# Kernel tuning notes

Hardware: AMD Instinct MI355X
Metric: run time of the kernel (lower is better)

## Reference

```python
import jax, jax.numpy as jnp
import numpy as np

L, D, H, FF, P, IMG, B = 6, 1024, 16, 4096, 14, 224, 16
S = (IMG // P) ** 2 + 1  # 257 tokens (CLS + patches)
DH = D // H
TOPK_RATIO, MOD_START, MOD_END = 0.8, 3, -2
EPS = 1e-5


def _ln(x, w, b):
    m = x.mean(-1, keepdims=True)
    v = ((x - m) ** 2).mean(-1, keepdims=True)
    return (x - m) * jax.lax.rsqrt(v + EPS) * w + b


def _quick_gelu(x):
    return x * jax.nn.sigmoid(1.702 * x)


def setup_inputs() -> dict:
    key = jax.random.key(0)
    ks = jax.random.split(key, 16)
    w = 0.02
    inp = {
        "pixel_values": jax.random.normal(ks[0], (B, 3, IMG, IMG), jnp.float32),
        "patch_w": jax.random.normal(ks[1], (D, 3, P, P), jnp.float32) * w,
        "class_emb": jax.random.normal(ks[2], (D,), jnp.float32) * w,
        "pos_emb": jax.random.normal(ks[3], (S, D), jnp.float32) * w,
        "ln1_w": jnp.ones((L, D), jnp.float32),
        "ln1_b": jnp.zeros((L, D), jnp.float32),
        "q_w": jax.random.normal(ks[4], (L, D, D), jnp.float32) * w,
        "q_b": jnp.zeros((L, D), jnp.float32),
        "k_w": jax.random.normal(ks[5], (L, D, D), jnp.float32) * w,
        "k_b": jnp.zeros((L, D), jnp.float32),
        "v_w": jax.random.normal(ks[6], (L, D, D), jnp.float32) * w,
        "v_b": jnp.zeros((L, D), jnp.float32),
        "o_w": jax.random.normal(ks[7], (L, D, D), jnp.float32) * w,
        "o_b": jnp.zeros((L, D), jnp.float32),
        "ln2_w": jnp.ones((L, D), jnp.float32),
        "ln2_b": jnp.zeros((L, D), jnp.float32),
        "fc1_w": jax.random.normal(ks[8], (L, FF, D), jnp.float32) * w,
        "fc1_b": jnp.zeros((L, FF), jnp.float32),
        "fc2_w": jax.random.normal(ks[9], (L, D, FF), jnp.float32) * w,
        "fc2_b": jnp.zeros((L, D), jnp.float32),
    }
    return inp


def reference(pixel_values, patch_w, class_emb, pos_emb,
              ln1_w, ln1_b, q_w, q_b, k_w, k_b, v_w, v_b, o_w, o_b,
              ln2_w, ln2_b, fc1_w, fc1_b, fc2_w, fc2_b):
    # --- CLIP vision embeddings (note: custom forward skips pre_layrnorm) ---
    feats = jax.lax.conv_general_dilated(
        pixel_values, patch_w, (P, P), 'VALID',
        dimension_numbers=('NCHW', 'OIHW', 'NCHW'))  # [B, D, 16, 16]
    feats = feats.reshape(B, D, -1).transpose(0, 2, 1)  # [B, 256, D]
    cls = jnp.broadcast_to(class_emb, (B, 1, D))
    x = jnp.concatenate([cls, feats], axis=1) + pos_emb[None]  # [B, S, D]

    scale = DH ** -0.5
    top_k = int(S * TOPK_RATIO)

    for idx in range(L):
        # --- CLIP encoder layer (pre-LN) ---
        res = x
        h = _ln(x, ln1_w[idx], ln1_b[idx])
        q = (h @ q_w[idx].T + q_b[idx]).reshape(B, S, H, DH)
        k = (h @ k_w[idx].T + k_b[idx]).reshape(B, S, H, DH)
        v = (h @ v_w[idx].T + v_b[idx]).reshape(B, S, H, DH)
        scores = jnp.einsum('bqhd,bkhd->bhqk', q, k) * scale
        attn = jax.nn.softmax(scores, axis=-1)  # [B, H, S, S]
        ctx = jnp.einsum('bhqk,bkhd->bqhd', attn, v).reshape(B, S, D)
        x = res + (ctx @ o_w[idx].T + o_b[idx])
        res = x
        h = _ln(x, ln2_w[idx], ln2_b[idx])
        h = _quick_gelu(h @ fc1_w[idx].T + fc1_b[idx])
        x = res + (h @ fc2_w[idx].T + fc2_b[idx])

        # --- MoD-style top-k selection + per-batch mask scatter ---
        if MOD_START <= idx <= L + MOD_END and (idx - MOD_START) % 2 == 0:
            aw = attn.mean(axis=1)                 # [B, S, S]
            sc = aw.sum(axis=2)                    # [B, S]
            sc = sc / sc.sum(axis=1, keepdims=True)
            _, top_idx = jax.lax.top_k(sc, top_k)  # [B, top_k]
            mask = jnp.zeros((B, S), bool).at[jnp.arange(B)[:, None], top_idx].set(True)
            # Original torch loop writes hidden_states back into a clone on both
            # mask and ~mask -> mathematically an identity copy.
            x = jnp.where(mask[:, :, None], x, x)

    return x


if __name__ == '__main__':
    out = reference(**setup_inputs())
    print(out.shape, out.dtype)
```

## Files before the change

### kernel.cpp

```cpp
#include <hip/hip_runtime.h>
#include <stdint.h>

typedef uint16_t u16;
typedef __attribute__((ext_vector_type(8))) short short8;
typedef __attribute__((ext_vector_type(4))) float f32x4;
typedef __attribute__((ext_vector_type(4))) u16 u16x4;

__device__ __forceinline__ u16 f2bf(float f) {
  union { float f; uint32_t i; } v; v.f = f;
  uint32_t r = v.i + 0x7fffu + ((v.i >> 16) & 1u);
  return (u16)(r >> 16);
}
__device__ __forceinline__ int imin(int a, int b) { return a < b ? a : b; }

#define GLD_LDS(gp, lp) __builtin_amdgcn_global_load_lds( \
    (__attribute__((address_space(1))) void*)(uintptr_t)(gp), \
    (__attribute__((address_space(3))) void*)(lp), 16, 0, 0)

#define BATCH 16
#define SEQ 257
#define DIM 1024
#define HEADS 16
#define DHEAD 64
#define FFDIM 4096
#define MROWS (BATCH * SEQ)
#define SPAD 288
#define KC 608

enum { EPI_PATCH = 0, EPI_QKV = 1, EPI_RES = 2, EPI_GELU = 3 };

struct GemmP {
  const u16* A; const u16* B;
  const float* bias;
  int lda, ldb, M, N, K;
  void* out;
  void* out2; void* out3;
  const float* aux;
};

template <int EPI, int MT>
__global__ __launch_bounds__(256) void gemm_bt(GemmP p) {
  constexpr int TM = MT * 32;
  constexpr int AISS = MT / 2;
  __shared__ __align__(16) u16 sA[TM * 32];
  __shared__ __align__(16) u16 sB[128 * 32];
  const int tid = threadIdx.x;
  const int w = tid >> 6, l = tid & 63, quad = l >> 4, lr = l & 15;
  const int wr = w >> 1, wc = w & 1;
  const int m0 = blockIdx.y * TM, n0 = blockIdx.x * 128;

  long aoff[AISS];
#pragma unroll
  for (int i = 0; i < AISS; ++i) {
    const int f = tid + i * 256;
    aoff[i] = (long)imin(m0 + (f >> 2), p.M - 1) * p.lda + ((f & 3) << 3);
  }
  long boff[2];
#pragma unroll
  for (int i = 0; i < 2; ++i) {
    const int f = tid + i * 256;
    boff[i] = (long)imin(n0 + (f >> 2), p.N - 1) * p.ldb + ((f & 3) << 3);
  }

  f32x4 acc[MT][4];
#pragma unroll
  for (int i = 0; i < MT; ++i)
#pragma unroll
    for (int j = 0; j < 4; ++j) acc[i][j] = (f32x4){0.f, 0.f, 0.f, 0.f};

  for (int k0 = 0; k0 < p.K; k0 += 32) {
    __syncthreads();
#pragma unroll
    for (int i = 0; i < AISS; ++i)
      GLD_LDS(p.A + aoff[i] + k0, &sA[(tid + i * 256) * 8]);
#pragma unroll
    for (int i = 0; i < 2; ++i)
      GLD_LDS(p.B + boff[i] + k0, &sB[(tid + i * 256) * 8]);
    __syncthreads();
    short8 af[MT], bg[4];
#pragma unroll
    for (int t = 0; t < MT; ++t)
      af[t] = *(const short8*)&sA[(wr * (MT * 16) + t * 16 + lr) * 32 + quad * 8];
#pragma unroll
    for (int t = 0; t < 4; ++t)
      bg[t] = *(const short8*)&sB[(wc * 64 + t * 16 + lr) * 32 + quad * 8];
#pragma unroll
    for (int mt = 0; mt < MT; ++mt)
#pragma unroll
      for (int nt = 0; nt < 4; ++nt)
        acc[mt][nt] = __builtin_amdgcn_mfma_f32_16x16x32_bf16(af[mt], bg[nt], acc[mt][nt], 0, 0, 0);
  }

#pragma unroll
  for (int mt = 0; mt < MT; ++mt) {
#pragma unroll
    for (int r = 0; r < 4; ++r) {
      const int gm = m0 + wr * (MT * 16) + mt * 16 + quad * 4 + r;
      if (gm >= p.M) continue;
#pragma unroll
      for (int nt = 0; nt < 4; ++nt) {
        const int gn = n0 + wc * 64 + nt * 16 + lr;
        if (gn >= p.N) continue;
        float v = acc[mt][nt][r];
        if (p.bias) v += p.bias[gn];
        if constexpr (EPI == EPI_PATCH) {
          const int b = gm >> 8, pp = gm & 255;
          ((float*)p.out)[((long)(b * SEQ + 1 + pp)) * DIM + gn] =
              v + p.aux[(1 + pp) * DIM + gn];
        } else if constexpr (EPI == EPI_QKV) {
          const int b = gm / SEQ, s = gm % SEQ;
          const int seg = gn >> 10, dloc = gn & 1023;
          const int h = dloc >> 6, dd = dloc & 63;
          const u16 val = f2bf(v);
          if (seg == 0)
            ((u16*)p.out)[(((long)(b * HEADS + h) * SEQ + s)) * DHEAD + dd] = val;
          else if (seg == 1)
            ((u16*)p.out2)[(((long)(b * HEADS + h) * SEQ + s)) * DHEAD + dd] = val;
          else
            ((u16*)p.out3)[((long)(b * HEADS + h) * DHEAD + dd) * SPAD + s] = val;
        } else if constexpr (EPI == EPI_RES) {
          float* o = (float*)p.out;
          o[(long)gm * p.N + gn] += v;
        } else if constexpr (EPI == EPI_GELU) {
          const float g = v / (1.f + __expf(-1.702f * v));
          ((u16*)p.out)[(long)gm * p.N + gn] = f2bf(g);
        }
      }
    }
  }
}

__global__ __launch_bounds__(256) void ln_k(const float* __restrict__ X,
                                            const float* __restrict__ w,
                                            const float* __restrict__ b,
                                            u16* __restrict__ O) {
  const int row = blockIdx.x, tid = threadIdx.x;
  const float4* xr = (const float4*)(X + (long)row * DIM);
  float4 v = xr[tid];
  float s = v.x + v.y + v.z + v.w;
  float s2 = v.x * v.x + v.y * v.y + v.z * v.z + v.w * v.w;
  for (int o = 32; o; o >>= 1) { s += __shfl_xor(s, o); s2 += __shfl_xor(s2, o); }
  __shared__ float red[8];
  const int wv = tid >> 6, l = tid & 63;
  if (l == 0) { red[wv] = s; red[4 + wv] = s2; }
  __syncthreads();
  s = red[0] + red[1] + red[2] + red[3];
  s2 = red[4] + red[5] + red[6] + red[7];
  const float mean = s * (1.f / DIM);
  const float var = s2 * (1.f / DIM) - mean * mean;
  const float rs = rsqrtf(var + 1e-5f);
  const int c = tid * 4;
  const float4 wv4 = *(const float4*)(w + c);
  const float4 bv4 = *(const float4*)(b + c);
  u16x4 o4;
  o4.x = f2bf((v.x - mean) * rs * wv4.x + bv4.x);
  o4.y = f2bf((v.y - mean) * rs * wv4.y + bv4.y);
  o4.z = f2bf((v.z - mean) * rs * wv4.z + bv4.z);
  o4.w = f2bf((v.w - mean) * rs * wv4.w + bv4.w);
  *(u16x4*)(O + (long)row * DIM + c) = o4;
}

__global__ __launch_bounds__(256) void attn_k(const u16* __restrict__ Q,
                                              const u16* __restrict__ Kx,
                                              const u16* __restrict__ Vt,
                                              u16* __restrict__ Ctx) {
  const int bh = blockIdx.x;
  const int q0 = blockIdx.y * 16;
  __shared__ float S[16][292];
  __shared__ __align__(16) u16 P[16][SPAD];
  const int tid = threadIdx.x, w = tid >> 6, l = tid & 63, quad = l >> 4, lr = l & 15;
  const u16* Qb = Q + (long)bh * SEQ * DHEAD;
  const u16* Kb = Kx + (long)bh * SEQ * DHEAD;
  const u16* Vb = Vt + (long)bh * DHEAD * SPAD;
  int qm = q0 + lr; if (qm > SEQ - 1) qm = SEQ - 1;
  const short8 aq0 = *(const short8*)(Qb + qm * DHEAD + quad * 8);
  const short8 aq1 = *(const short8*)(Qb + qm * DHEAD + 32 + quad * 8);
  for (int ct = 0; ct < 5; ++ct) {
    const int cn = ct * 64 + w * 16 + lr;
    const int cc = cn > SEQ - 1 ? SEQ - 1 : cn;
    const short8 b0 = *(const short8*)(Kb + cc * DHEAD + quad * 8);
    const short8 b1 = *(const short8*)(Kb + cc * DHEAD + 32 + quad * 8);
    f32x4 acc = (f32x4){0.f, 0.f, 0.f, 0.f};
    acc = __builtin_amdgcn_mfma_f32_16x16x32_bf16(aq0, b0, acc, 0, 0, 0);
    acc = __builtin_amdgcn_mfma_f32_16x16x32_bf16(aq1, b1, acc, 0, 0, 0);
    if (cn < SEQ) {
#pragma unroll
      for (int r = 0; r < 4; ++r) S[quad * 4 + r][cn] = acc[r] * 0.125f;
    }
  }
  __syncthreads();
#pragma unroll
  for (int rr = 0; rr < 4; ++rr) {
    const int m = w * 4 + rr;
    float mx = -1e30f;
    for (int c = l; c < SEQ; c += 64) mx = fmaxf(mx, S[m][c]);
    for (int o = 32; o; o >>= 1) mx = fmaxf(mx, __shfl_xor(mx, o));
    float sum = 0.f;
    for (int c = l; c < SEQ; c += 64) {
      const float e = __expf(S[m][c] - mx);
      S[m][c] = e;
      sum += e;
    }
    for (int o = 32; o; o >>= 1) sum += __shfl_xor(sum, o);
    const float inv = 1.f / sum;
    for (int c = l; c < SPAD; c += 64) P[m][c] = (c < SEQ) ? f2bf(S[m][c] * inv) : (u16)0;
  }
  __syncthreads();
  f32x4 acc = (f32x4){0.f, 0.f, 0.f, 0.f};
  for (int k0 = 0; k0 < SPAD; k0 += 32) {
    const short8 ap = *(const short8*)&P[lr][k0 + quad * 8];
    const short8 bv = *(const short8*)(Vb + (long)(w * 16 + lr) * SPAD + k0 + quad * 8);
    acc = __builtin_amdgcn_mfma_f32_16x16x32_bf16(ap, bv, acc, 0, 0, 0);
  }
  const int b = bh >> 4, h = bh & 15;
#pragma unroll
  for (int r = 0; r < 4; ++r) {
    const int q = q0 + quad * 4 + r;
    if (q < SEQ)
      Ctx[((long)(b * SEQ + q)) * DIM + h * DHEAD + w * 16 + lr] = f2bf(acc[r]);
  }
}

__global__ void f2b_k(const float* __restrict__ src, u16* __restrict__ dst, int n4) {
  const int i = blockIdx.x * 256 + threadIdx.x;
  if (i >= n4) return;
  const float4 v = ((const float4*)src)[i];
  u16x4 o;
  o.x = f2bf(v.x); o.y = f2bf(v.y); o.z = f2bf(v.z); o.w = f2bf(v.w);
  ((u16x4*)dst)[i] = o;
}

__global__ void cat3_k(const float* __restrict__ a, const float* __restrict__ b,
                       const float* __restrict__ c, float* __restrict__ o) {
  const int i = blockIdx.x * 256 + threadIdx.x;
  o[i] = (i < 1024) ? a[i] : (i < 2048 ? b[i - 1024] : c[i - 2048]);
}

__global__ void im2col_k(const float* __restrict__ pv, u16* __restrict__ out) {
  const long i = (long)blockIdx.x * 256 + threadIdx.x;
  if (i >= (long)4096 * KC) return;
  const int col = (int)(i % KC);
  const long row = i / KC;
  u16 val = 0;
  if (col < 588) {
    const int b = (int)(row >> 8), p = (int)(row & 255);
    const int py = p >> 4, px = p & 15;
    const int c = col / 196, rem = col % 196;
    const int ky = rem / 14, kx = rem % 14;
    val = f2bf(pv[(((long)b * 3 + c) * 224 + (py * 14 + ky)) * 224 + (px * 14 + kx)]);
  }
  out[i] = val;
}

__global__ void pwpad_k(const float* __restrict__ pw, u16* __restrict__ out) {
  const int i = blockIdx.x * 256 + threadIdx.x;
  if (i >= DIM * KC) return;
  const int col = i % KC, row = i / KC;
  out[i] = (col < 588) ? f2bf(pw[row * 588 + col]) : (u16)0;
}

__global__ void cls_k(const float* __restrict__ cls, const float* __restrict__ pos,
                      float* __restrict__ X) {
  const int i = blockIdx.x * 256 + threadIdx.x;
  const int b = i >> 10, d = i & 1023;
  X[((long)b * SEQ) * DIM + d] = cls[d] + pos[d];
}

__global__ void vtpad_k(u16* __restrict__ Vt) {
  const int i = blockIdx.x * 256 + threadIdx.x;
  if (i >= 256 * 64 * 31) return;
  const int dall = i / 31, s = SEQ + i % 31;
  Vt[(long)dall * SPAD + s] = 0;
}

__global__ void out_k(const float* __restrict__ X, float* __restrict__ O) {
  const int i = blockIdx.x * 256 + threadIdx.x;
  ((float4*)O)[i] = ((const float4*)X)[i];
}

#define OFF_X 0L
#define OFF_H 16842752L
#define OFF_Q 25264128L
#define OFF_K 33685504L
#define OFF_VT 42106880L
#define OFF_CTX 51544064L
#define OFF_FF 59965440L
#define OFF_W 93650944L
#define OFF_B3 (OFF_W + 6291456L)
#define OFF_IM OFF_FF
#define OFF_PW (OFF_FF + 4980736L)

extern "C" void kernel_launch(void* const* d_in, const int* in_sizes, int n_in,
                              void* d_out, int out_size, void* d_ws, size_t ws_size,
                              hipStream_t stream) {
  const float* pv = (const float*)d_in[0];
  const float* patch_w = (const float*)d_in[1];
  const float* class_emb = (const float*)d_in[2];
  const float* pos_emb = (const float*)d_in[3];
  const float* ln1_w = (const float*)d_in[4];
  const float* ln1_b = (const float*)d_in[5];
  const float* q_w = (const float*)d_in[6];
  const float* q_b = (const float*)d_in[7];
  const float* k_w = (const float*)d_in[8];
  const float* k_b = (const float*)d_in[9];
  const float* v_w = (const float*)d_in[10];
  const float* v_b = (const float*)d_in[11];
  const float* o_w = (const float*)d_in[12];
  const float* o_b = (const float*)d_in[13];
  const float* ln2_w = (const float*)d_in[14];
  const float* ln2_b = (const float*)d_in[15];
  const float* fc1_w = (const float*)d_in[16];
  const float* fc1_b = (const float*)d_in[17];
  const float* fc2_w = (const float*)d_in[18];
  const float* fc2_b = (const float*)d_in[19];

  char* ws = (char*)d_ws;
  float* X = (float*)(ws + OFF_X);
  u16* Hb = (u16*)(ws + OFF_H);
  u16* Qb = (u16*)(ws + OFF_Q);
  u16* Kb = (u16*)(ws + OFF_K);
  u16* Vt = (u16*)(ws + OFF_VT);
  u16* Ctx = (u16*)(ws + OFF_CTX);
  u16* FFh = (u16*)(ws + OFF_FF);
  u16* Wb = (u16*)(ws + OFF_W);
  float* B3 = (float*)(ws + OFF_B3);
  u16* Im = (u16*)(ws + OFF_IM);
  u16* Pw = (u16*)(ws + OFF_PW);

  const int NSQ4 = DIM * DIM / 4;
  const int NFF4 = FFDIM * DIM / 4;
  const int GSQ = (NSQ4 + 255) / 256, GFF = (NFF4 + 255) / 256;

  im2col_k<<<(4096 * KC + 255) / 256, 256, 0, stream>>>(pv, Im);
  pwpad_k<<<(DIM * KC + 255) / 256, 256, 0, stream>>>(patch_w, Pw);
  cls_k<<<(BATCH * DIM) / 256, 256, 0, stream>>>(class_emb, pos_emb, X);
  vtpad_k<<<(256 * 64 * 31 + 255) / 256, 256, 0, stream>>>(Vt);
  {
    GemmP g = {};
    g.A = Im; g.lda = KC; g.B = Pw; g.ldb = KC; g.bias = nullptr;
    g.M = 4096; g.N = DIM; g.K = KC; g.out = X; g.aux = pos_emb;
    gemm_bt<EPI_PATCH, 2><<<dim3(8, 64, 1), 256, 0, stream>>>(g);
  }

  for (int idx = 0; idx < 6; ++idx) {
    ln_k<<<MROWS, 256, 0, stream>>>(X, ln1_w + idx * DIM, ln1_b + idx * DIM, Hb);
    {
      f2b_k<<<GSQ, 256, 0, stream>>>(q_w + (long)idx * DIM * DIM, Wb, NSQ4);
      f2b_k<<<GSQ, 256, 0, stream>>>(k_w + (long)idx * DIM * DIM, Wb + DIM * DIM, NSQ4);
      f2b_k<<<GSQ, 256, 0, stream>>>(v_w + (long)idx * DIM * DIM, Wb + 2 * DIM * DIM, NSQ4);
      cat3_k<<<12, 256, 0, stream>>>(q_b + idx * DIM, k_b + idx * DIM, v_b + idx * DIM, B3);
      GemmP g = {};
      g.A = Hb; g.lda = DIM; g.B = Wb; g.ldb = DIM; g.bias = B3;
      g.M = MROWS; g.N = 3 * DIM; g.K = DIM;
      g.out = Qb; g.out2 = Kb; g.out3 = Vt;
      gemm_bt<EPI_QKV, 4><<<dim3(24, 33, 1), 256, 0, stream>>>(g);
    }
    attn_k<<<dim3(256, 17, 1), 256, 0, stream>>>(Qb, Kb, Vt, Ctx);
    {
      GemmP g = {};
      f2b_k<<<GSQ, 256, 0, stream>>>(o_w + (long)idx * DIM * DIM, Wb, NSQ4);
      g.A = Ctx; g.lda = DIM; g.B = Wb; g.ldb = DIM;
      g.bias = o_b + idx * DIM; g.M = MROWS; g.N = DIM; g.K = DIM; g.out = X;
      gemm_bt<EPI_RES, 2><<<dim3(8, 65, 1), 256, 0, stream>>>(g);
    }
    ln_k<<<MROWS, 256, 0, stream>>>(X, ln2_w + idx * DIM, ln2_b + idx * DIM, Hb);
    {
      GemmP g = {};
      f2b_k<<<GFF, 256, 0, stream>>>(fc1_w + (long)idx * FFDIM * DIM, Wb, NFF4);
      g.A = Hb; g.lda = DIM; g.B = Wb; g.ldb = DIM;
      g.bias = fc1_b + idx * FFDIM; g.M = MROWS; g.N = FFDIM; g.K = DIM; g.out = FFh;
      gemm_bt<EPI_GELU, 4><<<dim3(32, 33, 1), 256, 0, stream>>>(g);
    }
    {
      GemmP g = {};
      f2b_k<<<GFF, 256, 0, stream>>>(fc2_w + (long)idx * DIM * FFDIM, Wb, NFF4);
      g.A = FFh; g.lda = FFDIM; g.B = Wb; g.ldb = FFDIM;
      g.bias = fc2_b + idx * DIM; g.M = MROWS; g.N = DIM; g.K = FFDIM; g.out = X;
      gemm_bt<EPI_RES, 2><<<dim3(8, 65, 1), 256, 0, stream>>>(g);
    }
  }
  out_k<<<(MROWS * DIM / 4) / 256, 256, 0, stream>>>(X, (float*)d_out);
}
```

Measured before the change: 2.571 ms.

## Double GEMM K-step to 64 with two-panel LDS tiles; fuse QKV weight conversion

The GEMM main loop now loads a 64-wide K slab per iteration, stored as two 32-column panels in shared memory, and issues two MFMAs per accumulator between barriers. This halves the number of barrier pairs and load-issue rounds per K, at the cost of doubled LDS use, which may reduce occupancy. The patch-embedding K padding grows from 608 to 640 so it divides by 64, which adds a little extra zero work. The three separate Q/K/V weight conversion launches are merged into a single kernel.

New measurement: 2.560 ms. Within noise of the previous version (-0.5%).

```diff
diff --git a/kernel.cpp b/kernel.cpp
--- a/kernel.cpp
+++ b/kernel.cpp
@@ -25,7 +25,7 @@
 #define FFDIM 4096
 #define MROWS (BATCH * SEQ)
 #define SPAD 288
-#define KC 608
+#define KC 640
 
 enum { EPI_PATCH = 0, EPI_QKV = 1, EPI_RES = 2, EPI_GELU = 3 };
 
@@ -41,25 +41,28 @@
 template <int EPI, int MT>
 __global__ __launch_bounds__(256) void gemm_bt(GemmP p) {
   constexpr int TM = MT * 32;
-  constexpr int AISS = MT / 2;
-  __shared__ __align__(16) u16 sA[TM * 32];
-  __shared__ __align__(16) u16 sB[128 * 32];
+  constexpr int NA = TM / 32;
+  constexpr int SHA = (MT == 4) ? 9 : 8;
+  __shared__ __align__(16) u16 sA[2][TM][32];
+  __shared__ __align__(16) u16 sB[2][128][32];
   const int tid = threadIdx.x;
   const int w = tid >> 6, l = tid & 63, quad = l >> 4, lr = l & 15;
   const int wr = w >> 1, wc = w & 1;
   const int m0 = blockIdx.y * TM, n0 = blockIdx.x * 128;
 
-  long aoff[AISS];
-#pragma unroll
-  for (int i = 0; i < AISS; ++i) {
+  long aoff[NA];
+#pragma unroll
+  for (int i = 0; i < NA; ++i) {
     const int f = tid + i * 256;
-    aoff[i] = (long)imin(m0 + (f >> 2), p.M - 1) * p.lda + ((f & 3) << 3);
-  }
-  long boff[2];
-#pragma unroll
-  for (int i = 0; i < 2; ++i) {
+    const int pnl = f >> SHA, r = (f >> 2) & (TM - 1), s = f & 3;
+    aoff[i] = (long)imin(m0 + r, p.M - 1) * p.lda + pnl * 32 + s * 8;
+  }
+  long boff[4];
+#pragma unroll
+  for (int i = 0; i < 4; ++i) {
     const int f = tid + i * 256;
-    boff[i] = (long)imin(n0 + (f >> 2), p.N - 1) * p.ldb + ((f & 3) << 3);
+    const int pnl = f >> 9, r = (f >> 2) & 127, s = f & 3;
+    boff[i] = (long)imin(n0 + r, p.N - 1) * p.ldb + pnl * 32 + s * 8;
   }
 
   f32x4 acc[MT][4];
@@ -68,27 +71,33 @@
 #pragma unroll
     for (int j = 0; j < 4; ++j) acc[i][j] = (f32x4){0.f, 0.f, 0.f, 0.f};
 
-  for (int k0 = 0; k0 < p.K; k0 += 32) {
+  for (int k0 = 0; k0 < p.K; k0 += 64) {
     __syncthreads();
 #pragma unroll
-    for (int i = 0; i < AISS; ++i)
-      GLD_LDS(p.A + aoff[i] + k0, &sA[(tid + i * 256) * 8]);
-#pragma unroll
-    for (int i = 0; i < 2; ++i)
-      GLD_LDS(p.B + boff[i] + k0, &sB[(tid + i * 256) * 8]);
+    for (int i = 0; i < NA; ++i)
+      GLD_LDS(p.A + aoff[i] + k0, (u16*)sA + (tid + i * 256) * 8);
+#pragma unroll
+    for (int i = 0; i < 4; ++i)
+      GLD_LDS(p.B + boff[i] + k0, (u16*)sB + (tid + i * 256) * 8);
     __syncthreads();
-    short8 af[MT], bg[4];
-#pragma unroll
-    for (int t = 0; t < MT; ++t)
-      af[t] = *(const short8*)&sA[(wr * (MT * 16) + t * 16 + lr) * 32 + quad * 8];
-#pragma unroll
-    for (int t = 0; t < 4; ++t)
-      bg[t] = *(const short8*)&sB[(wc * 64 + t * 16 + lr) * 32 + quad * 8];
+    short8 a0[MT], a1[MT], b0[4], b1[4];
+#pragma unroll
+    for (int t = 0; t < MT; ++t) {
+      a0[t] = *(const short8*)&sA[0][wr * (MT * 16) + t * 16 + lr][quad * 8];
+      a1[t] = *(const short8*)&sA[1][wr * (MT * 16) + t * 16 + lr][quad * 8];
+    }
+#pragma unroll
+    for (int t = 0; t < 4; ++t) {
+      b0[t] = *(const short8*)&sB[0][wc * 64 + t * 16 + lr][quad * 8];
+      b1[t] = *(const short8*)&sB[1][wc * 64 + t * 16 + lr][quad * 8];
+    }
 #pragma unroll
     for (int mt = 0; mt < MT; ++mt)
 #pragma unroll
-      for (int nt = 0; nt < 4; ++nt)
-        acc[mt][nt] = __builtin_amdgcn_mfma_f32_16x16x32_bf16(af[mt], bg[nt], acc[mt][nt], 0, 0, 0);
+      for (int nt = 0; nt < 4; ++nt) {
+        acc[mt][nt] = __builtin_amdgcn_mfma_f32_16x16x32_bf16(a0[mt], b0[nt], acc[mt][nt], 0, 0, 0);
+        acc[mt][nt] = __builtin_amdgcn_mfma_f32_16x16x32_bf16(a1[mt], b1[nt], acc[mt][nt], 0, 0, 0);
+      }
   }
 
 #pragma unroll
@@ -230,6 +239,20 @@
   ((u16x4*)dst)[i] = o;
 }
 
+__global__ void wcvt3_k(const float* __restrict__ q, const float* __restrict__ k,
+                        const float* __restrict__ v, u16* __restrict__ dst, int n4) {
+  const int i = blockIdx.x * 256 + threadIdx.x;
+  if (i >= 3 * n4) return;
+  const float* src; int j;
+  if (i < n4) { src = q; j = i; }
+  else if (i < 2 * n4) { src = k; j = i - n4; }
+  else { src = v; j = i - 2 * n4; }
+  const float4 vv = ((const float4*)src)[j];
+  u16x4 o;
+  o.x = f2bf(vv.x); o.y = f2bf(vv.y); o.z = f2bf(vv.z); o.w = f2bf(vv.w);
+  ((u16x4*)dst)[i] = o;
+}
+
 __global__ void cat3_k(const float* __restrict__ a, const float* __restrict__ b,
                        const float* __restrict__ c, float* __restrict__ o) {
   const int i = blockIdx.x * 256 + threadIdx.x;
@@ -288,7 +311,7 @@
 #define OFF_W 93650944L
 #define OFF_B3 (OFF_W + 6291456L)
 #define OFF_IM OFF_FF
-#define OFF_PW (OFF_FF + 4980736L)
+#define OFF_PW (OFF_FF + 5242880L)
 
 extern "C" void kernel_launch(void* const* d_in, const int* in_sizes, int n_in,
                               void* d_out, int out_size, void* d_ws, size_t ws_size,
@@ -345,9 +368,9 @@
   for (int idx = 0; idx < 6; ++idx) {
     ln_k<<<MROWS, 256, 0, stream>>>(X, ln1_w + idx * DIM, ln1_b + idx * DIM, Hb);
     {
-      f2b_k<<<GSQ, 256, 0, stream>>>(q_w + (long)idx * DIM * DIM, Wb, NSQ4);
-      f2b_k<<<GSQ, 256, 0, stream>>>(k_w + (long)idx * DIM * DIM, Wb + DIM * DIM, NSQ4);
-      f2b_k<<<GSQ, 256, 0, stream>>>(v_w + (long)idx * DIM * DIM, Wb + 2 * DIM * DIM, NSQ4);
+      wcvt3_k<<<(3 * NSQ4 + 255) / 256, 256, 0, stream>>>(
+          q_w + (long)idx * DIM * DIM, k_w + (long)idx * DIM * DIM,
+          v_w + (long)idx * DIM * DIM, Wb, NSQ4);
       cat3_k<<<12, 256, 0, stream>>>(q_b + idx * DIM, k_b + idx * DIM, v_b + idx * DIM, B3);
       GemmP g = {};
       g.A = Hb; g.lda = DIM; g.B = Wb; g.ldb = DIM; g.bias = B3;
```
